# Optimization experiments

Measured on AMD Instinct MI355X. Metric: run time of the kernel, lower is better.

## Reference

```python
import jax, jax.numpy as jnp
import numpy as np

B, N = 65536, 8
OBS0, OBS1, OBS2 = 6, 1024, 7
H, HC, NA = 64, 128, 2


def _glorot(key, shape):
    fan_in = shape[0]
    lim = 1.0 / np.sqrt(fan_in)
    return jax.random.uniform(key, shape, jnp.float32, -lim, lim)


def setup_inputs() -> dict:
    key = jax.random.key(0)
    ks = jax.random.split(key, 24)
    state0 = jax.random.normal(ks[0], (B, OBS0), jnp.float32)
    state1 = jax.random.normal(ks[1], (B, OBS1), jnp.float32)
    state2 = jax.random.normal(ks[2], (B, N, OBS2), jnp.float32)
    keep = (jax.random.uniform(ks[3], (B, N, 1)) > 0.35) | (jnp.arange(N)[None, :, None] == 0)
    state2 = state2 * keep.astype(jnp.float32)
    return {
        "state0": state0, "state1": state1, "state2": state2,
        "W0": _glorot(ks[4], (OBS0, H)), "b0": jnp.zeros((H,), jnp.float32),
        "Wg": _glorot(ks[5], (OBS1, H)), "bg": jnp.zeros((H,), jnp.float32),
        "Ws1": _glorot(ks[6], (OBS2, H)), "bs1": jnp.zeros((H,), jnp.float32),
        "Ws2": _glorot(ks[7], (H, H)), "bs2": jnp.zeros((H,), jnp.float32),
        "Wq": _glorot(ks[8], (H, H)),
        "Wk": _glorot(ks[9], (H, H)),
        "Wv": _glorot(ks[10], (H, H)),
        "Wc1": _glorot(ks[11], (3 * H, HC)), "bc1": jnp.zeros((HC,), jnp.float32),
        "Wc2": _glorot(ks[12], (HC, HC)), "bc2": jnp.zeros((HC,), jnp.float32),
        "Wc3": _glorot(ks[13], (HC, NA)), "bc3": jnp.zeros((NA,), jnp.float32),
    }


def reference(state0, state1, state2,
              W0, b0, Wg, bg, Ws1, bs1, Ws2, bs2,
              Wq, Wk, Wv, Wc1, bc1, Wc2, bc2, Wc3, bc3):
    own_e = jax.nn.relu(state0 @ W0 + b0)                      # [B, 64]
    env_e = jax.nn.relu(state1 @ Wg + bg)                      # [B, 64]
    intru_e = jax.nn.relu(state2 @ Ws1 + bs1)                  # [B, N, 64]
    intru_e = jax.nn.relu(intru_e @ Ws2 + bs2)                 # [B, N, 64]

    q = own_e @ Wq                                             # [B, 64]
    k = intru_e @ Wk                                           # [B, N, 64]
    v = intru_e @ Wv                                           # [B, N, 64]

    # mask: True where the neighbor slot is non-padding (mean over feats != 0)
    mask = jnp.mean(state2, axis=2, keepdims=True) != 0        # [B, N, 1] bool

    score = jnp.einsum('bnd,bd->bn', k, q)[..., None]          # [B, N, 1]
    score_m = jnp.where(mask, score, -jnp.inf)
    alpha = jax.nn.softmax(score_m / np.sqrt(H), axis=1)       # [B, N, 1]
    alpha_m = jnp.where(mask, alpha, 0.0)
    v_att = jnp.sum(v * alpha_m, axis=1)                       # [B, 64]

    concat = jnp.concatenate((own_e, env_e, v_att), axis=1)    # [B, 192]
    h = jax.nn.relu(concat @ Wc1 + bc1)
    h = jax.nn.relu(h @ Wc2 + bc2)
    return jnp.tanh(h @ Wc3 + bc3)                             # [B, n_actions]
```

## Files before the change

kernel.cpp:

```cpp
#include <hip/hip_runtime.h>
#include <math.h>


typedef float f32x4 __attribute__((ext_vector_type(4)));
typedef float f32x4u __attribute__((ext_vector_type(4), aligned(4)));
typedef float f32x2u __attribute__((ext_vector_type(2), aligned(4)));
typedef __bf16 bf16x8 __attribute__((ext_vector_type(8)));
typedef unsigned short u16x8 __attribute__((ext_vector_type(8)));

#define DI __device__ __forceinline__

DI unsigned short f2bf_u(float f) {
  unsigned u = __builtin_bit_cast(unsigned, f);
  u += 0x7fffu + ((u >> 16) & 1u);
  return (unsigned short)(u >> 16);
}
DI float bfu2f(unsigned short s) {
  unsigned u = ((unsigned)s) << 16;
  return __builtin_bit_cast(float, u);
}
DI u16x8 cvt8(f32x4 x, f32x4 y) {
  bf16x8 r;
  r[0] = (__bf16)x[0]; r[1] = (__bf16)x[1]; r[2] = (__bf16)x[2]; r[3] = (__bf16)x[3];
  r[4] = (__bf16)y[0]; r[5] = (__bf16)y[1]; r[6] = (__bf16)y[2]; r[7] = (__bf16)y[3];
  return __builtin_bit_cast(u16x8, r);
}
DI f32x4 mfma16(u16x8 a, u16x8 b, f32x4 c) {
  return __builtin_amdgcn_mfma_f32_16x16x32_bf16(
      __builtin_bit_cast(bf16x8, a), __builtin_bit_cast(bf16x8, b), c, 0, 0, 0);
}


constexpr size_t WS_WGF = 0;
constexpr size_t WS_WS2 = 131072;
constexpr size_t WS_WV  = 139264;
constexpr size_t WS_MQK = 147456;
constexpr size_t WS_WC1 = 155648;
constexpr size_t WS_WC2 = 204800;

__global__ __launch_bounds__(256) void k_prep(
    const float* __restrict__ Wg, const float* __restrict__ Ws2,
    const float* __restrict__ Wv, const float* __restrict__ Wq,
    const float* __restrict__ Wk, const float* __restrict__ Wc1,
    const float* __restrict__ Wc2,
    unsigned short* __restrict__ wgf, unsigned short* __restrict__ ws2f,
    unsigned short* __restrict__ wvf, unsigned short* __restrict__ mqkf,
    unsigned short* __restrict__ wc1f, unsigned short* __restrict__ wc2f) {
  const int idx = blockIdx.x * 256 + threadIdx.x;
  const float* src = nullptr;
  unsigned short* dst;
  int i, ntm, NC;
  bool is_mqk = false;
  if (idx < 65536)      { src = Wg;  dst = wgf;  i = idx;          ntm = 2; NC = 64;  }
  else if (idx < 69632) { src = Ws2; dst = ws2f; i = idx - 65536;  ntm = 2; NC = 64;  }
  else if (idx < 73728) { src = Wv;  dst = wvf;  i = idx - 69632;  ntm = 2; NC = 64;  }
  else if (idx < 77824) { is_mqk = true; dst = mqkf; i = idx - 73728; ntm = 2; NC = 64; }
  else if (idx < 102400){ src = Wc1; dst = wc1f; i = idx - 77824;  ntm = 3; NC = 128; }
  else                  { src = Wc2; dst = wc2f; i = idx - 102400; ntm = 3; NC = 128; }
  const int j = i & 7, ln = (i >> 3) & 63, t2 = i >> 9;
  const int nt = t2 & ((1 << ntm) - 1), kt = t2 >> ntm;
  const int k = kt * 32 + (ln >> 4) * 8 + j, n = nt * 16 + (ln & 15);
  float val;
  if (is_mqk) {
    const f32x4* qp = (const f32x4*)(Wq + k * 64);
    const f32x4* kp = (const f32x4*)(Wk + n * 64);
    float acc = 0.f;
#pragma unroll
    for (int d4 = 0; d4 < 16; ++d4) {
      const f32x4 a = qp[d4], b = kp[d4];
#pragma unroll
      for (int e = 0; e < 4; ++e) acc = fmaf(a[e], b[e], acc);
    }
    val = acc;
  } else {
    val = src[k * NC + n];
  }
  dst[i] = f2bf_u(val);
}

__global__ __launch_bounds__(256, 3) void k_main(
    const float* __restrict__ s0, const float* __restrict__ s1,
    const float* __restrict__ s2,
    const float* __restrict__ W0, const float* __restrict__ b0v,
    const float* __restrict__ bg,
    const float* __restrict__ Ws1, const float* __restrict__ bs1,
    const unsigned short* __restrict__ ws2f, const float* __restrict__ bs2,
    const unsigned short* __restrict__ wvf, const unsigned short* __restrict__ mqkf,
    const unsigned short* __restrict__ wc1f, const float* __restrict__ bc1,
    const unsigned short* __restrict__ wc2f, const float* __restrict__ bc2,
    const float* __restrict__ Wc3, const float* __restrict__ bc3,
    const unsigned short* __restrict__ wgf,
    float* __restrict__ out) {
  __shared__ __align__(16) char smem[54272];
  u16x8* EF = (u16x8*)smem;
  unsigned short* EFs = (unsigned short*)smem;
  u16x8* H1F = (u16x8*)smem;
  unsigned short* H1Fs = (unsigned short*)smem;
  float* H2 = (float*)(smem + 8192);
  u16x8* CF = (u16x8*)(smem + 32768);
  unsigned short* CFs = (unsigned short*)(smem + 32768);
  float* QK = (float*)(smem + 45056);
  f32x4* RED4 = (f32x4*)(smem + 45056);
  u16x8* SEF = (u16x8*)(smem + 45056);
  float* SC = (float*)(smem + 53248);

  const int tid = threadIdx.x;
  const int lane = tid & 63, wave = tid >> 6;
  const int lo = lane & 15, q = lane >> 4;
  const int bbase = blockIdx.x * 32;

  const int bl8 = tid >> 3, n8 = tid & 7;
  const float* s2p = s2 + ((size_t)(bbase + bl8) * 8 + n8) * 7;
  const f32x4u x03 = *(const f32x4u*)s2p;
  const f32x2u x45 = *(const f32x2u*)(s2p + 4);
  const float x6 = s2p[6];
  const float* s0p = s0 + (size_t)(bbase + bl8) * 6;
  const f32x4u y03 = *(const f32x4u*)s0p;
  const f32x2u y45 = *(const f32x2u*)(s0p + 4);

  const int p = wave & 1, emt = wave >> 1;
  {
    const float* arow =
        s1 + (size_t)(bbase + emt * 16 + lo) * 1024 + p * 512 + q * 8;
    const u16x8* wp = (const u16x8*)wgf + p * 4096 + lane;
    f32x4 acc0 = {}, acc1 = {}, acc2 = {}, acc3 = {};
    f32x4 a0 = *(const f32x4*)arow, a1 = *(const f32x4*)(arow + 4);
    u16x8 b0 = wp[0], b1 = wp[64], b2 = wp[128], b3 = wp[192];
    for (int ks = 0; ks < 16; ++ks) {
      const f32x4 ca0 = a0, ca1 = a1;
      const u16x8 cb0 = b0, cb1 = b1, cb2 = b2, cb3 = b3;
      if (ks < 15) {
        const float* ap = arow + (ks + 1) * 32;
        a0 = *(const f32x4*)ap;
        a1 = *(const f32x4*)(ap + 4);
        const u16x8* bp = wp + (ks + 1) * 256;
        b0 = bp[0]; b1 = bp[64]; b2 = bp[128]; b3 = bp[192];
      }
      const u16x8 af = cvt8(ca0, ca1);
      acc0 = mfma16(af, cb0, acc0);
      acc1 = mfma16(af, cb1, acc1);
      acc2 = mfma16(af, cb2, acc2);
      acc3 = mfma16(af, cb3, acc3);
    }
    if (p) {
      RED4[0 * 128 + emt * 64 + lane] = acc0;
      RED4[1 * 128 + emt * 64 + lane] = acc1;
      RED4[2 * 128 + emt * 64 + lane] = acc2;
      RED4[3 * 128 + emt * 64 + lane] = acc3;
    }
    __syncthreads();
    if (!p) {
      acc0 += RED4[0 * 128 + emt * 64 + lane];
      acc1 += RED4[1 * 128 + emt * 64 + lane];
      acc2 += RED4[2 * 128 + emt * 64 + lane];
      acc3 += RED4[3 * 128 + emt * 64 + lane];
      const f32x4 av[4] = {acc0, acc1, acc2, acc3};
#pragma unroll
      for (int nt = 0; nt < 4; ++nt) {
        const float bias = bg[nt * 16 + lo];
        const int h = nt * 16 + lo;
#pragma unroll
        for (int ri = 0; ri < 4; ++ri) {
          const float v = fmaxf(av[nt][ri] + bias, 0.f);
          CFs[((emt * 6 + 2 + (h >> 5)) * 64 +
               ((((h >> 3) & 3) << 4) | (q * 4 + ri))) * 8 + (h & 7)] = f2bf_u(v);
        }
      }
    }
  }

  bool maskreg;
  {
    float xv[7] = {x03[0], x03[1], x03[2], x03[3], x45[0], x45[1], x6};
    const float sum = xv[0] + xv[1] + xv[2] + xv[3] + xv[4] + xv[5] + xv[6];
    maskreg = (sum != 0.f);
    const int mt = tid >> 4, rl = tid & 15;
#pragma unroll
    for (int c = 0; c < 8; ++c) {
      float a[8];
#pragma unroll
      for (int i = 0; i < 8; ++i) a[i] = bs1[c * 8 + i];
#pragma unroll
      for (int j = 0; j < 7; ++j) {
        const float* wr = Ws1 + j * 64 + c * 8;
#pragma unroll
        for (int i = 0; i < 8; ++i) a[i] = fmaf(xv[j], wr[i], a[i]);
      }
      u16x8 pk;
#pragma unroll
      for (int i = 0; i < 8; ++i) pk[i] = f2bf_u(fmaxf(a[i], 0.f));
      EF[(mt * 2 + (c >> 2)) * 64 + (((c & 3) << 4) | rl)] = pk;
    }
  }
  __syncthreads();

  {
    u16x8 Bf[4][2];
#pragma unroll
    for (int nt = 0; nt < 4; ++nt)
#pragma unroll
      for (int kt = 0; kt < 2; ++kt)
        Bf[nt][kt] = ((const u16x8*)ws2f)[(kt * 4 + nt) * 64 + lane];
    float bias[4];
#pragma unroll
    for (int nt = 0; nt < 4; ++nt) bias[nt] = bs2[nt * 16 + lo];
#pragma unroll
    for (int mi = 0; mi < 4; ++mi) {
      const int mt = wave * 4 + mi;
      const u16x8 A0 = EF[(mt * 2 + 0) * 64 + lane];
      const u16x8 A1 = EF[(mt * 2 + 1) * 64 + lane];
      f32x4 acc[4] = {};
#pragma unroll
      for (int nt = 0; nt < 4; ++nt) {
        acc[nt] = mfma16(A0, Bf[nt][0], acc[nt]);
        acc[nt] = mfma16(A1, Bf[nt][1], acc[nt]);
      }
#pragma unroll
      for (int nt = 0; nt < 4; ++nt) {
        const int h = nt * 16 + lo;
#pragma unroll
        for (int ri = 0; ri < 4; ++ri) {
          const float v = fmaxf(acc[nt][ri] + bias[nt], 0.f);
          const int rr = mt * 16 + q * 4 + ri;
          EFs[((mt * 2 + (h >> 5)) * 64 + ((((h >> 3) & 3) << 4) | (rr & 15))) * 8 +
              (h & 7)] = f2bf_u(v);
        }
      }
    }
  }
  __syncthreads();

  {
    const int mt = bl8 >> 4, fl = ((n8 & 3) << 4) | (bl8 & 15), kt = n8 >> 2;
    const float yv[6] = {y03[0], y03[1], y03[2], y03[3], y45[0], y45[1]};
    float a[8];
#pragma unroll
    for (int i = 0; i < 8; ++i) a[i] = b0v[n8 * 8 + i];
#pragma unroll
    for (int j = 0; j < 6; ++j) {
      const float* wr = W0 + j * 64 + n8 * 8;
#pragma unroll
      for (int i = 0; i < 8; ++i) a[i] = fmaf(yv[j], wr[i], a[i]);
    }
    u16x8 pk;
#pragma unroll
    for (int i = 0; i < 8; ++i) pk[i] = f2bf_u(fmaxf(a[i], 0.f));
    CF[(mt * 6 + kt) * 64 + fl] = pk;
  }
  __syncthreads();

  {
#pragma unroll
    for (int pp = 0; pp < 2; ++pp) {
      const int pr = wave * 2 + pp, mt = pr >> 2, nt = pr & 3;
      const u16x8 A0 = CF[(mt * 6 + 0) * 64 + lane];
      const u16x8 A1 = CF[(mt * 6 + 1) * 64 + lane];
      const u16x8 B0 = ((const u16x8*)mqkf)[(0 * 4 + nt) * 64 + lane];
      const u16x8 B1 = ((const u16x8*)mqkf)[(1 * 4 + nt) * 64 + lane];
      f32x4 acc = {};
      acc = mfma16(A0, B0, acc);
      acc = mfma16(A1, B1, acc);
#pragma unroll
      for (int ri = 0; ri < 4; ++ri)
        QK[(mt * 16 + q * 4 + ri) * 64 + nt * 16 + lo] = acc[ri];
    }
  }
  __syncthreads();

  {
    const int r = tid, bl = r >> 3, mt = r >> 4, rl = r & 15;
    float dot = 0.f;
#pragma unroll
    for (int c = 0; c < 8; ++c) {
      const u16x8 e = EF[(mt * 2 + (c >> 2)) * 64 + (((c & 3) << 4) | rl)];
      const float* qkp = QK + bl * 64 + c * 8;
      const f32x4 qa = *(const f32x4*)(qkp);
      const f32x4 qb = *(const f32x4*)(qkp + 4);
#pragma unroll
      for (int i = 0; i < 4; ++i) dot = fmaf(bfu2f(e[i]), qa[i], dot);
#pragma unroll
      for (int i = 0; i < 4; ++i) dot = fmaf(bfu2f(e[4 + i]), qb[i], dot);
    }
    SC[r] = maskreg ? dot * 0.125f : -1e30f;
  }
  __syncthreads();

  if (tid < 32) {
    float s[8];
#pragma unroll
    for (int n = 0; n < 8; ++n) s[n] = SC[tid * 8 + n];
    float mx = s[0];
#pragma unroll
    for (int n = 1; n < 8; ++n) mx = fmaxf(mx, s[n]);
    float e[8], sum = 0.f;
#pragma unroll
    for (int n = 0; n < 8; ++n) { e[n] = __expf(s[n] - mx); sum += e[n]; }
    const float inv = 1.f / sum;
#pragma unroll
    for (int n = 0; n < 8; ++n) SC[tid * 8 + n] = e[n] * inv;
  }
  __syncthreads();

  {
    float al[8];
#pragma unroll
    for (int n = 0; n < 8; ++n) al[n] = SC[bl8 * 8 + n];
    float a[8] = {0.f, 0.f, 0.f, 0.f, 0.f, 0.f, 0.f, 0.f};
#pragma unroll
    for (int n = 0; n < 8; ++n) {
      const int rr = bl8 * 8 + n;
      const u16x8 e =
          EF[((rr >> 4) * 2 + (n8 >> 2)) * 64 + (((n8 & 3) << 4) | (rr & 15))];
#pragma unroll
      for (int i = 0; i < 8; ++i) a[i] = fmaf(al[n], bfu2f(e[i]), a[i]);
    }
    u16x8 pk;
#pragma unroll
    for (int i = 0; i < 8; ++i) pk[i] = f2bf_u(a[i]);
    SEF[((bl8 >> 4) * 2 + (n8 >> 2)) * 64 + (((n8 & 3) << 4) | (bl8 & 15))] = pk;
  }
  __syncthreads();

  {
#pragma unroll
    for (int pp = 0; pp < 2; ++pp) {
      const int pr = wave * 2 + pp, mt = pr >> 2, nt = pr & 3;
      const u16x8 A0 = SEF[(mt * 2 + 0) * 64 + lane];
      const u16x8 A1 = SEF[(mt * 2 + 1) * 64 + lane];
      const u16x8 B0 = ((const u16x8*)wvf)[(0 * 4 + nt) * 64 + lane];
      const u16x8 B1 = ((const u16x8*)wvf)[(1 * 4 + nt) * 64 + lane];
      f32x4 acc = {};
      acc = mfma16(A0, B0, acc);
      acc = mfma16(A1, B1, acc);
      const int h = nt * 16 + lo;
#pragma unroll
      for (int ri = 0; ri < 4; ++ri) {
        const int rr = mt * 16 + q * 4 + ri;
        CFs[((mt * 6 + 4 + (h >> 5)) * 64 + ((((h >> 3) & 3) << 4) | (rr & 15))) * 8 +
            (h & 7)] = f2bf_u(acc[ri]);
      }
    }
  }
  __syncthreads();

  {
    const int mt = wave & 1, ntb = (wave >> 1) * 4;
    u16x8 A[6];
#pragma unroll
    for (int kt = 0; kt < 6; ++kt) A[kt] = CF[(mt * 6 + kt) * 64 + lane];
#pragma unroll
    for (int ni = 0; ni < 4; ++ni) {
      const int nt = ntb + ni;
      f32x4 acc = {};
#pragma unroll
      for (int kt = 0; kt < 6; ++kt) {
        const u16x8 Bf = ((const u16x8*)wc1f)[(kt * 8 + nt) * 64 + lane];
        acc = mfma16(A[kt], Bf, acc);
      }
      const float bias = bc1[nt * 16 + lo];
      const int h = nt * 16 + lo;
#pragma unroll
      for (int ri = 0; ri < 4; ++ri) {
        const float v = fmaxf(acc[ri] + bias, 0.f);
        const int rr = mt * 16 + q * 4 + ri;
        H1Fs[((mt * 4 + (h >> 5)) * 64 + ((((h >> 3) & 3) << 4) | (rr & 15))) * 8 +
             (h & 7)] = f2bf_u(v);
      }
    }
  }
  __syncthreads();

  {
    const int mt = wave & 1, ntb = (wave >> 1) * 4;
    u16x8 A[4];
#pragma unroll
    for (int kt = 0; kt < 4; ++kt) A[kt] = H1F[(mt * 4 + kt) * 64 + lane];
#pragma unroll
    for (int ni = 0; ni < 4; ++ni) {
      const int nt = ntb + ni;
      f32x4 acc = {};
#pragma unroll
      for (int kt = 0; kt < 4; ++kt) {
        const u16x8 Bf = ((const u16x8*)wc2f)[(kt * 8 + nt) * 64 + lane];
        acc = mfma16(A[kt], Bf, acc);
      }
      const float bias = bc2[nt * 16 + lo];
#pragma unroll
      for (int ri = 0; ri < 4; ++ri)
        H2[(mt * 16 + q * 4 + ri) * 132 + nt * 16 + lo] =
            fmaxf(acc[ri] + bias, 0.f);
    }
  }
  __syncthreads();

  {
    const int kq = n8 >> 1, a = n8 & 1;
    const f32x4* h4 = (const f32x4*)(H2 + bl8 * 132 + kq * 32);
    const float* wr = Wc3 + kq * 64;
    float acc = 0.f;
#pragma unroll
    for (int j4 = 0; j4 < 8; ++j4) {
      const f32x4 hv = h4[j4];
#pragma unroll
      for (int e = 0; e < 4; ++e) acc = fmaf(hv[e], wr[(j4 * 4 + e) * 2 + a], acc);
    }
    acc += __shfl_down(acc, 2);
    acc += __shfl_down(acc, 4);
    if (kq == 0) out[(size_t)(bbase + bl8) * 2 + a] = tanhf(acc + bc3[a]);
  }
}

extern "C" void kernel_launch(void* const* d_in, const int* in_sizes, int n_in,
                              void* d_out, int out_size, void* d_ws, size_t ws_size,
                              hipStream_t stream) {
  const float* s0  = (const float*)d_in[0];
  const float* s1  = (const float*)d_in[1];
  const float* s2  = (const float*)d_in[2];
  const float* W0  = (const float*)d_in[3];
  const float* b0  = (const float*)d_in[4];
  const float* Wg  = (const float*)d_in[5];
  const float* bg  = (const float*)d_in[6];
  const float* Ws1 = (const float*)d_in[7];
  const float* bs1 = (const float*)d_in[8];
  const float* Ws2 = (const float*)d_in[9];
  const float* bs2 = (const float*)d_in[10];
  const float* Wq  = (const float*)d_in[11];
  const float* Wk  = (const float*)d_in[12];
  const float* Wv  = (const float*)d_in[13];
  const float* Wc1 = (const float*)d_in[14];
  const float* bc1 = (const float*)d_in[15];
  const float* Wc2 = (const float*)d_in[16];
  const float* bc2 = (const float*)d_in[17];
  const float* Wc3 = (const float*)d_in[18];
  const float* bc3 = (const float*)d_in[19];

  char* ws = (char*)d_ws;
  unsigned short* wgf  = (unsigned short*)(ws + WS_WGF);
  unsigned short* ws2f = (unsigned short*)(ws + WS_WS2);
  unsigned short* wvf  = (unsigned short*)(ws + WS_WV);
  unsigned short* mqkf = (unsigned short*)(ws + WS_MQK);
  unsigned short* wc1f = (unsigned short*)(ws + WS_WC1);
  unsigned short* wc2f = (unsigned short*)(ws + WS_WC2);

  hipLaunchKernelGGL(k_prep, dim3(464), dim3(256), 0, stream, Wg, Ws2, Wv, Wq,
                     Wk, Wc1, Wc2, wgf, ws2f, wvf, mqkf, wc1f, wc2f);
  hipLaunchKernelGGL(k_main, dim3(2048), dim3(256), 0, stream, s0, s1, s2, W0,
                     b0, bg, Ws1, bs1, ws2f, bs2, wvf, mqkf, wc1f, bc1, wc2f,
                     bc2, Wc3, bc3, wgf, (float*)d_out);
}
```

Before: 458.6 us.

## Split env GEMM into separate kernel with async LDS-staged state1 loads

Moves the large state1 @ Wg projection out of the fused main kernel into its own kernel. The new kernel streams state1 into double-buffered, XOR-swizzled shared memory using global_load_lds, then feeds MFMA from LDS. It writes bf16 env embeddings to a workspace buffer that the remaining kernel reads back. The aim is better bandwidth and occupancy on the dominant 256 MB read, at the cost of an extra launch and a small intermediate round trip through global memory.

```diff
diff --git a/kernel.cpp b/kernel.cpp
--- a/kernel.cpp
+++ b/kernel.cpp
@@ -28,6 +28,11 @@
 DI f32x4 mfma16(u16x8 a, u16x8 b, f32x4 c) {
   return __builtin_amdgcn_mfma_f32_16x16x32_bf16(
       __builtin_bit_cast(bf16x8, a), __builtin_bit_cast(bf16x8, b), c, 0, 0, 0);
+}
+DI void gload_lds16(const void* g, void* l) {
+  typedef __attribute__((address_space(1))) const unsigned GU;
+  typedef __attribute__((address_space(3))) unsigned LU;
+  __builtin_amdgcn_global_load_lds((GU*)g, (LU*)l, 16, 0, 0);
 }
 
 
@@ -37,6 +42,7 @@
 constexpr size_t WS_MQK = 147456;
 constexpr size_t WS_WC1 = 155648;
 constexpr size_t WS_WC2 = 204800;
+constexpr size_t WS_ENV = 237568;
 
 __global__ __launch_bounds__(256) void k_prep(
     const float* __restrict__ Wg, const float* __restrict__ Ws2,
@@ -78,18 +84,95 @@
   dst[i] = f2bf_u(val);
 }
 
-__global__ __launch_bounds__(256, 3) void k_main(
-    const float* __restrict__ s0, const float* __restrict__ s1,
-    const float* __restrict__ s2,
+__global__ __launch_bounds__(256, 4) void k_env(
+    const float* __restrict__ s1, const unsigned short* __restrict__ wgf,
+    const float* __restrict__ bg, unsigned short* __restrict__ envf) {
+  __shared__ __align__(16) char smem[36864];
+  unsigned short* STGs = (unsigned short*)(smem + 32768);
+  u16x8* STG = (u16x8*)(smem + 32768);
+
+  const int tid = threadIdx.x;
+  const int lane = tid & 63, wave = tid >> 6;
+  const int lo = lane & 15, q = lane >> 4;
+  const int bbase = blockIdx.x * 32;
+  const int mt = wave & 1, ntb = wave >> 1;
+
+  const char* s1b = (const char*)(s1 + (size_t)bbase * 1024);
+
+  int srow[4], scol[4];
+#pragma unroll
+  for (int i = 0; i < 4; ++i) {
+    const int T = (i * 256 + tid) * 16;
+    srow[i] = T >> 9;
+    scol[i] = (T & 511) ^ ((srow[i] & 7) << 4);
+  }
+  auto stage = [&](char* dst, int c) {
+    const int srcb = c * 512;
+#pragma unroll
+    for (int i = 0; i < 4; ++i)
+      gload_lds16(s1b + (size_t)srow[i] * 4096 + srcb + scol[i],
+                  dst + (i * 256 + tid) * 16);
+  };
+
+  f32x4 acc0 = {}, acc1 = {};
+  const int row = mt * 16 + lo;
+  const int sw = (row & 7) << 4;
+  const u16x8* wgfp = (const u16x8*)wgf + (ntb * 2) * 64 + lane;
+
+  auto compute = [&](const char* src, int c) {
+#pragma unroll
+    for (int kt = 0; kt < 4; ++kt) {
+      const int base = row * 512 + kt * 128 + q * 32;
+      const f32x4 alo = *(const f32x4*)(src + (base ^ sw));
+      const f32x4 ahi = *(const f32x4*)(src + ((base + 16) ^ sw));
+      const int ktg = c * 4 + kt;
+      const u16x8 b0 = wgfp[(ktg * 4 + 0) * 64];
+      const u16x8 b1 = wgfp[(ktg * 4 + 1) * 64];
+      const u16x8 af = cvt8(alo, ahi);
+      acc0 = mfma16(af, b0, acc0);
+      acc1 = mfma16(af, b1, acc1);
+    }
+  };
+
+  stage(smem, 0);
+  __syncthreads();
+#pragma unroll
+  for (int cc = 0; cc < 4; ++cc) {
+    stage(smem + 16384, cc * 2 + 1);
+    compute(smem, cc * 2);
+    __syncthreads();
+    if (cc < 3) stage(smem, cc * 2 + 2);
+    compute(smem + 16384, cc * 2 + 1);
+    __syncthreads();
+  }
+
+#pragma unroll
+  for (int ni = 0; ni < 2; ++ni) {
+    const f32x4 a = ni ? acc1 : acc0;
+    const int h = (ntb * 2 + ni) * 16 + lo;
+    const float bias = bg[h];
+#pragma unroll
+    for (int ri = 0; ri < 4; ++ri) {
+      const float v = fmaxf(a[ri] + bias, 0.f);
+      STGs[((mt * 2 + ntb) * 64 + ((((h >> 3) & 3) << 4) | (q * 4 + ri))) * 8 +
+           (h & 7)] = f2bf_u(v);
+    }
+  }
+  __syncthreads();
+  const u16x8 v = STG[(mt * 2 + ntb) * 64 + lane];
+  *((u16x8*)envf + ((size_t)((bbase >> 4) + mt) * 2 + ntb) * 64 + lane) = v;
+}
+
+__global__ __launch_bounds__(256, 3) void k_rest(
+    const float* __restrict__ s0, const float* __restrict__ s2,
     const float* __restrict__ W0, const float* __restrict__ b0v,
-    const float* __restrict__ bg,
     const float* __restrict__ Ws1, const float* __restrict__ bs1,
     const unsigned short* __restrict__ ws2f, const float* __restrict__ bs2,
     const unsigned short* __restrict__ wvf, const unsigned short* __restrict__ mqkf,
     const unsigned short* __restrict__ wc1f, const float* __restrict__ bc1,
     const unsigned short* __restrict__ wc2f, const float* __restrict__ bc2,
     const float* __restrict__ Wc3, const float* __restrict__ bc3,
-    const unsigned short* __restrict__ wgf,
+    const unsigned short* __restrict__ envf,
     float* __restrict__ out) {
   __shared__ __align__(16) char smem[54272];
   u16x8* EF = (u16x8*)smem;
@@ -98,9 +181,7 @@
   unsigned short* H1Fs = (unsigned short*)smem;
   float* H2 = (float*)(smem + 8192);
   u16x8* CF = (u16x8*)(smem + 32768);
-  unsigned short* CFs = (unsigned short*)(smem + 32768);
   float* QK = (float*)(smem + 45056);
-  f32x4* RED4 = (f32x4*)(smem + 45056);
   u16x8* SEF = (u16x8*)(smem + 45056);
   float* SC = (float*)(smem + 53248);
 
@@ -108,6 +189,10 @@
   const int lane = tid & 63, wave = tid >> 6;
   const int lo = lane & 15, q = lane >> 4;
   const int bbase = blockIdx.x * 32;
+
+  const int emt_ = wave >> 1, ekt = wave & 1;
+  const u16x8 ev =
+      *((const u16x8*)envf + ((size_t)((bbase >> 4) + emt_) * 2 + ekt) * 64 + lane);
 
   const int bl8 = tid >> 3, n8 = tid & 7;
   const float* s2p = s2 + ((size_t)(bbase + bl8) * 8 + n8) * 7;
@@ -118,56 +203,7 @@
   const f32x4u y03 = *(const f32x4u*)s0p;
   const f32x2u y45 = *(const f32x2u*)(s0p + 4);
 
-  const int p = wave & 1, emt = wave >> 1;
-  {
-    const float* arow =
-        s1 + (size_t)(bbase + emt * 16 + lo) * 1024 + p * 512 + q * 8;
-    const u16x8* wp = (const u16x8*)wgf + p * 4096 + lane;
-    f32x4 acc0 = {}, acc1 = {}, acc2 = {}, acc3 = {};
-    f32x4 a0 = *(const f32x4*)arow, a1 = *(const f32x4*)(arow + 4);
-    u16x8 b0 = wp[0], b1 = wp[64], b2 = wp[128], b3 = wp[192];
-    for (int ks = 0; ks < 16; ++ks) {
-      const f32x4 ca0 = a0, ca1 = a1;
-      const u16x8 cb0 = b0, cb1 = b1, cb2 = b2, cb3 = b3;
-      if (ks < 15) {
-        const float* ap = arow + (ks + 1) * 32;
-        a0 = *(const f32x4*)ap;
-        a1 = *(const f32x4*)(ap + 4);
-        const u16x8* bp = wp + (ks + 1) * 256;
-        b0 = bp[0]; b1 = bp[64]; b2 = bp[128]; b3 = bp[192];
-      }
-      const u16x8 af = cvt8(ca0, ca1);
-      acc0 = mfma16(af, cb0, acc0);
-      acc1 = mfma16(af, cb1, acc1);
-      acc2 = mfma16(af, cb2, acc2);
-      acc3 = mfma16(af, cb3, acc3);
-    }
-    if (p) {
-      RED4[0 * 128 + emt * 64 + lane] = acc0;
-      RED4[1 * 128 + emt * 64 + lane] = acc1;
-      RED4[2 * 128 + emt * 64 + lane] = acc2;
-      RED4[3 * 128 + emt * 64 + lane] = acc3;
-    }
-    __syncthreads();
-    if (!p) {
-      acc0 += RED4[0 * 128 + emt * 64 + lane];
-      acc1 += RED4[1 * 128 + emt * 64 + lane];
-      acc2 += RED4[2 * 128 + emt * 64 + lane];
-      acc3 += RED4[3 * 128 + emt * 64 + lane];
-      const f32x4 av[4] = {acc0, acc1, acc2, acc3};
-#pragma unroll
-      for (int nt = 0; nt < 4; ++nt) {
-        const float bias = bg[nt * 16 + lo];
-        const int h = nt * 16 + lo;
-#pragma unroll
-        for (int ri = 0; ri < 4; ++ri) {
-          const float v = fmaxf(av[nt][ri] + bias, 0.f);
-          CFs[((emt * 6 + 2 + (h >> 5)) * 64 +
-               ((((h >> 3) & 3) << 4) | (q * 4 + ri))) * 8 + (h & 7)] = f2bf_u(v);
-        }
-      }
-    }
-  }
+  CF[(emt_ * 6 + 2 + ekt) * 64 + lane] = ev;
 
   bool maskreg;
   {
@@ -322,6 +358,7 @@
   __syncthreads();
 
   {
+    unsigned short* CFs = (unsigned short*)CF;
 #pragma unroll
     for (int pp = 0; pp < 2; ++pp) {
       const int pr = wave * 2 + pp, mt = pr >> 2, nt = pr & 3;
@@ -441,10 +478,12 @@
   unsigned short* mqkf = (unsigned short*)(ws + WS_MQK);
   unsigned short* wc1f = (unsigned short*)(ws + WS_WC1);
   unsigned short* wc2f = (unsigned short*)(ws + WS_WC2);
+  unsigned short* envf = (unsigned short*)(ws + WS_ENV);
 
   hipLaunchKernelGGL(k_prep, dim3(464), dim3(256), 0, stream, Wg, Ws2, Wv, Wq,
                      Wk, Wc1, Wc2, wgf, ws2f, wvf, mqkf, wc1f, wc2f);
-  hipLaunchKernelGGL(k_main, dim3(2048), dim3(256), 0, stream, s0, s1, s2, W0,
-                     b0, bg, Ws1, bs1, ws2f, bs2, wvf, mqkf, wc1f, bc1, wc2f,
-                     bc2, Wc3, bc3, wgf, (float*)d_out);
-}
+  hipLaunchKernelGGL(k_env, dim3(2048), dim3(256), 0, stream, s1, wgf, bg, envf);
+  hipLaunchKernelGGL(k_rest, dim3(2048), dim3(256), 0, stream, s0, s2, W0, b0,
+                     Ws1, bs1, ws2f, bs2, wvf, mqkf, wc1f, bc1, wc2f, bc2, Wc3,
+                     bc3, envf, (float*)d_out);
+}
```

Measured after the change: 470.7 us. 2.7% more time.
